# Kernel tuning notes

Hardware: AMD Instinct MI355X
Metric: run time of the kernel (lower is better)

## Reference

```python
import jax, jax.numpy as jnp
import numpy as np

B, S, E, H = 16, 256, 4096, 16
D = E // H  # 256; module's matmul pattern requires S == D and B == H


def setup_inputs() -> dict:
    rng = jax.random.key(0)
    k0, k1, k2, k3, k4 = jax.random.split(rng, 5)
    return {
        "query": jax.random.normal(k0, (B, S, E), jnp.float32),
        "key": jax.random.normal(k1, (B, S, E), jnp.float32),
        "value": jax.random.normal(k2, (B, S, E), jnp.float32),
        # out_proj: torch nn.Linear(E, E) -> y = x @ W.T + b
        "out_w": jax.random.normal(k3, (E, E), jnp.float32) * 0.02,
        "out_b": jnp.zeros((E,), jnp.float32),
    }


def reference(query, key, value, out_w, out_b):
    scale = D ** -0.5
    # split heads: [B, S, E] -> [B, H, S, D]
    q = (query * scale).reshape(B, S, H, D).transpose(0, 2, 1, 3)
    k = key.reshape(B, S, H, D).transpose(0, 2, 1, 3)
    v = value.reshape(B, S, H, D).transpose(0, 2, 1, 3)
    # torch.matmul(q_head, k_head) with NO transpose: contracts q's D with k's S
    # (valid because S == D). aw: [B, H, S, D]
    aw = jnp.einsum('bhit,bhtj->bhij', q, k)
    # attn_weights.transpose(0, 1): [B, H, ...] -> [H, B, ...]
    aw = jnp.swapaxes(aw, 0, 1)
    # eval mode path: softmax over last dim (no dropout)
    aw = jax.nn.softmax(aw, axis=-1)
    # torch.matmul(aw [H,B,S,D], v [B,H,S,D]): batch dims broadcast because B == H,
    # pairing elementwise -> out[x,y] = aw[x,y] @ v[x,y]
    out = jnp.einsum('xyit,xytj->xyij', aw, v)
    # transpose(1, 2) then reshape to (B, S, E)
    out = jnp.swapaxes(out, 1, 2).reshape(B, S, E)
    # out_proj
    return out @ out_w.T + out_b
```

## Files before the change

kernel.cpp:

```cpp
#include <hip/hip_runtime.h>

#define AS1 __attribute__((address_space(1)))
#define AS3 __attribute__((address_space(3)))

typedef __bf16 bf16x8 __attribute__((ext_vector_type(8)));
typedef float f32x4 __attribute__((ext_vector_type(4)));

__device__ __forceinline__ unsigned short f2bf(float f) {
  unsigned int u = __builtin_bit_cast(unsigned int, f);
  u += 0x7fffu + ((u >> 16) & 1u);
  return (unsigned short)(u >> 16);
}

__global__ __launch_bounds__(256) void kv_transpose(
    const float* __restrict__ key, const float* __restrict__ value,
    unsigned short* __restrict__ KT2, unsigned short* __restrict__ VT2) {
  __shared__ float tr[32 * 33];
  const int tid = threadIdx.x;
  const int ts  = blockIdx.y;
  const int pp  = blockIdx.x >> 3;
  const int s   = blockIdx.x & 7;
  const int b   = ts ? (pp >> 4) : (pp & 15);
  const int h   = ts ? (pp & 15) : (pp >> 4);
  const float* src = (ts ? value : key) + ((size_t)(b * 256 + s * 32)) * 4096 + h * 256;
  unsigned short* dst = (ts ? VT2 : KT2) + (size_t)(pp * 8 + s) * 8192;
  const int tt = tid >> 3;
  const int q8 = tid & 7;
  for (int jb = 0; jb < 8; ++jb) {
    float4 v = *(const float4*)(src + (size_t)tt * 4096 + jb * 32 + q8 * 4);
    tr[tt * 33 + q8 * 4 + 0] = v.x;
    tr[tt * 33 + q8 * 4 + 1] = v.y;
    tr[tt * 33 + q8 * 4 + 2] = v.z;
    tr[tt * 33 + q8 * 4 + 3] = v.w;
    __syncthreads();
    ushort4 o;
    o.x = f2bf(tr[(q8 * 4 + 0) * 33 + tt]);
    o.y = f2bf(tr[(q8 * 4 + 1) * 33 + tt]);
    o.z = f2bf(tr[(q8 * 4 + 2) * 33 + tt]);
    o.w = f2bf(tr[(q8 * 4 + 3) * 33 + tt]);
    *(ushort4*)(dst + (jb * 32 + tt) * 32 + q8 * 4) = o;
    __syncthreads();
  }
}

__global__ __launch_bounds__(256, 2) void attn_kernel(
    const float* __restrict__ qin, const unsigned short* __restrict__ KT2,
    const unsigned short* __restrict__ VT2, unsigned short* __restrict__ attn) {
  __shared__ __align__(16) unsigned short kv[8192];
  __shared__ __align__(16) unsigned short plds[4 * 16 * 264];

  const int tid  = threadIdx.x;
  const int lane = tid & 63;
  const int wave = tid >> 6;
  const int li   = lane & 15;
  const int ks   = lane >> 4;

  const int bid = blockIdx.x;
  const int pp  = (bid & 7) * 32 + ((bid >> 3) & 31);
  const int ib  = bid >> 8;
  const int x = pp >> 4, y = pp & 15;
  const int i0 = ib * 64 + wave * 16;

  bf16x8 qf[8];
  {
    const float* qrow = qin + ((size_t)(y * 256 + i0 + li)) * 4096 + x * 256 + ks * 8;
#pragma unroll
    for (int s = 0; s < 8; ++s) {
      float4 v0 = *(const float4*)(qrow + s * 32);
      float4 v1 = *(const float4*)(qrow + s * 32 + 4);
      union { bf16x8 v; unsigned short u[8]; } t;
      t.u[0] = f2bf(v0.x * 0.0625f); t.u[1] = f2bf(v0.y * 0.0625f);
      t.u[2] = f2bf(v0.z * 0.0625f); t.u[3] = f2bf(v0.w * 0.0625f);
      t.u[4] = f2bf(v1.x * 0.0625f); t.u[5] = f2bf(v1.y * 0.0625f);
      t.u[6] = f2bf(v1.z * 0.0625f); t.u[7] = f2bf(v1.w * 0.0625f);
      qf[s] = t.v;
    }
  }

  const f32x4 vzero = {0.f, 0.f, 0.f, 0.f};
  f32x4 sacc[16];
#pragma unroll
  for (int f = 0; f < 16; ++f) sacc[f] = vzero;

  const unsigned short* ktile = KT2 + (size_t)pp * 65536;
#pragma unroll
  for (int s = 0; s < 8; ++s) {
    __syncthreads();
#pragma unroll
    for (int cc = 0; cc < 4; ++cc) {
      const unsigned short* g = ktile + (size_t)s * 8192 + (cc * 256 + tid) * 8;
      __builtin_amdgcn_global_load_lds((AS1 unsigned int*)g,
          (AS3 unsigned int*)((AS3 char*)kv + cc * 4096 + wave * 1024), 16, 0, 0);
    }
    __syncthreads();
#pragma unroll
    for (int f = 0; f < 16; ++f) {
      bf16x8 bfr = *(const bf16x8*)&kv[(f * 16 + li) * 32 + ks * 8];
      sacc[f] = __builtin_amdgcn_mfma_f32_16x16x32_bf16(qf[s], bfr, sacc[f], 0, 0, 0);
    }
  }

  float sm[4];
#pragma unroll
  for (int qi = 0; qi < 4; ++qi) {
    float m = sacc[0][qi];
#pragma unroll
    for (int f = 1; f < 16; ++f) m = fmaxf(m, sacc[f][qi]);
    m = fmaxf(m, __shfl_xor(m, 1));
    m = fmaxf(m, __shfl_xor(m, 2));
    m = fmaxf(m, __shfl_xor(m, 4));
    m = fmaxf(m, __shfl_xor(m, 8));
    float ssum = 0.f;
#pragma unroll
    for (int f = 0; f < 16; ++f) {
      float pv = __expf(sacc[f][qi] - m);
      sacc[f][qi] = pv;
      ssum += pv;
    }
    ssum += __shfl_xor(ssum, 1);
    ssum += __shfl_xor(ssum, 2);
    ssum += __shfl_xor(ssum, 4);
    ssum += __shfl_xor(ssum, 8);
    sm[qi] = ssum;
  }

  unsigned short* pw = plds + wave * 4224;
#pragma unroll
  for (int f = 0; f < 16; ++f)
#pragma unroll
    for (int qi = 0; qi < 4; ++qi)
      pw[(ks * 4 + qi) * 264 + f * 16 + li] = f2bf(sacc[f][qi]);

  f32x4 oacc[16];
#pragma unroll
  for (int f = 0; f < 16; ++f) oacc[f] = vzero;
  const unsigned short* vtile = VT2 + (size_t)pp * 65536;
  const unsigned short* pr = plds + wave * 4224 + li * 264;
#pragma unroll
  for (int s2 = 0; s2 < 8; ++s2) {
    __syncthreads();
#pragma unroll
    for (int cc = 0; cc < 4; ++cc) {
      const unsigned short* g = vtile + (size_t)s2 * 8192 + (cc * 256 + tid) * 8;
      __builtin_amdgcn_global_load_lds((AS1 unsigned int*)g,
          (AS3 unsigned int*)((AS3 char*)kv + cc * 4096 + wave * 1024), 16, 0, 0);
    }
    __syncthreads();
    bf16x8 afr = *(const bf16x8*)&pr[s2 * 32 + ks * 8];
#pragma unroll
    for (int f = 0; f < 16; ++f) {
      bf16x8 bfr = *(const bf16x8*)&kv[(f * 16 + li) * 32 + ks * 8];
      oacc[f] = __builtin_amdgcn_mfma_f32_16x16x32_bf16(afr, bfr, oacc[f], 0, 0, 0);
    }
  }

  float rs4[4];
#pragma unroll
  for (int qi = 0; qi < 4; ++qi) rs4[qi] = 1.0f / sm[qi];
  unsigned short* abase = attn + (size_t)(x * 256 + i0 + ks * 4) * 4096 + y * 256 + li;
#pragma unroll
  for (int f = 0; f < 16; ++f)
#pragma unroll
    for (int qi = 0; qi < 4; ++qi)
      abase[(size_t)qi * 4096 + f * 16] = f2bf(oacc[f][qi] * rs4[qi]);
}

__global__ __launch_bounds__(256) void convw(const float* __restrict__ w,
                                             unsigned short* __restrict__ o) {
  const int i = blockIdx.x * 256 + threadIdx.x;
  const float4* s = (const float4*)w + (size_t)i * 2;
  float4 v0 = s[0], v1 = s[1];
  uint4 pk;
  pk.x = (unsigned)f2bf(v0.x) | ((unsigned)f2bf(v0.y) << 16);
  pk.y = (unsigned)f2bf(v0.z) | ((unsigned)f2bf(v0.w) << 16);
  pk.z = (unsigned)f2bf(v1.x) | ((unsigned)f2bf(v1.y) << 16);
  pk.w = (unsigned)f2bf(v1.z) | ((unsigned)f2bf(v1.w) << 16);
  *((uint4*)o + i) = pk;
}

__global__ __launch_bounds__(256, 2) void proj_gemm(
    const unsigned short* __restrict__ A, const unsigned short* __restrict__ W,
    const float* __restrict__ bias, float* __restrict__ out) {
  __shared__ __align__(16) unsigned short As[4096];
  __shared__ __align__(16) unsigned short Bs[4096];
  const int tid  = threadIdx.x;
  const int lane = tid & 63;
  const int wave = tid >> 6;
  const int li   = lane & 15;
  const int ks   = lane >> 4;
  const int wr = wave >> 1, wc = wave & 1;

  const int bid = blockIdx.x;
  const int swz = (bid & 7) * 128 + (bid >> 3);
  const int m0 = (swz >> 5) * 128, n0 = (swz & 31) * 128;

  const f32x4 vzero = {0.f, 0.f, 0.f, 0.f};
  f32x4 acc[4][4];
#pragma unroll
  for (int m = 0; m < 4; ++m)
#pragma unroll
    for (int n = 0; n < 4; ++n) acc[m][n] = vzero;

  const char* a0 = (const char*)A + (size_t)(m0 + (tid >> 2)) * 8192 + (tid & 3) * 16;
  const char* a1 = a0 + (size_t)64 * 8192;
  const char* b0 = (const char*)W + (size_t)(n0 + (tid >> 2)) * 8192 + (tid & 3) * 16;
  const char* b1 = b0 + (size_t)64 * 8192;
  AS3 unsigned int* lA0 = (AS3 unsigned int*)((AS3 char*)As + wave * 1024);
  AS3 unsigned int* lA1 = (AS3 unsigned int*)((AS3 char*)As + 4096 + wave * 1024);
  AS3 unsigned int* lB0 = (AS3 unsigned int*)((AS3 char*)Bs + wave * 1024);
  AS3 unsigned int* lB1 = (AS3 unsigned int*)((AS3 char*)Bs + 4096 + wave * 1024);

  for (int kt = 0; kt < 128; ++kt) {
    __builtin_amdgcn_global_load_lds((AS1 unsigned int*)(a0 + kt * 64), lA0, 16, 0, 0);
    __builtin_amdgcn_global_load_lds((AS1 unsigned int*)(a1 + kt * 64), lA1, 16, 0, 0);
    __builtin_amdgcn_global_load_lds((AS1 unsigned int*)(b0 + kt * 64), lB0, 16, 0, 0);
    __builtin_amdgcn_global_load_lds((AS1 unsigned int*)(b1 + kt * 64), lB1, 16, 0, 0);
    __syncthreads();
    bf16x8 af[4], bf[4];
#pragma unroll
    for (int m = 0; m < 4; ++m)
      af[m] = *(const bf16x8*)&As[(wr * 64 + m * 16 + li) * 32 + ks * 8];
#pragma unroll
    for (int n = 0; n < 4; ++n)
      bf[n] = *(const bf16x8*)&Bs[(wc * 64 + n * 16 + li) * 32 + ks * 8];
#pragma unroll
    for (int m = 0; m < 4; ++m)
#pragma unroll
      for (int n = 0; n < 4; ++n)
        acc[m][n] = __builtin_amdgcn_mfma_f32_16x16x32_bf16(af[m], bf[n], acc[m][n], 0, 0, 0);
    __syncthreads();
  }

  float bv[4];
#pragma unroll
  for (int n = 0; n < 4; ++n) bv[n] = bias[n0 + wc * 64 + n * 16 + li];
#pragma unroll
  for (int m = 0; m < 4; ++m) {
#pragma unroll
    for (int qi = 0; qi < 4; ++qi) {
      const int row = m0 + wr * 64 + m * 16 + ks * 4 + qi;
      float* orow = out + (size_t)row * 4096 + n0 + wc * 64 + li;
#pragma unroll
      for (int n = 0; n < 4; ++n) orow[n * 16] = acc[m][n][qi] + bv[n];
    }
  }
}

extern "C" void kernel_launch(void* const* d_in, const int* in_sizes, int n_in,
                              void* d_out, int out_size, void* d_ws, size_t ws_size,
                              hipStream_t stream) {
  const float* q = (const float*)d_in[0];
  const float* k = (const float*)d_in[1];
  const float* v = (const float*)d_in[2];
  const float* w = (const float*)d_in[3];
  const float* b = (const float*)d_in[4];
  float* out = (float*)d_out;
  char* ws = (char*)d_ws;

  unsigned short* attn = (unsigned short*)ws;
  unsigned short* KT2  = (unsigned short*)(ws + (size_t)33554432);
  unsigned short* VT2  = (unsigned short*)(ws + (size_t)67108864);
  unsigned short* wbf  = KT2;

  kv_transpose<<<dim3(2048, 2), 256, 0, stream>>>(k, v, KT2, VT2);
  attn_kernel<<<1024, 256, 0, stream>>>(q, KT2, VT2, attn);
  convw<<<8192, 256, 0, stream>>>(w, wbf);
  proj_gemm<<<1024, 256, 0, stream>>>(attn, wbf, b, out);
}
```

Measured before the change: 276.2 us.

## Rewrite output projection GEMM as 256x256 tile, 8-wave, double-buffered pipeline

Replaces the 128x128, 4-wave projection GEMM with a 256x256-tile, 8-wave kernel. It uses a 128 KB LDS double buffer with async global-to-LDS prefetch two k-steps ahead, an XOR-swizzled LDS layout to avoid bank conflicts, and interleaves MFMA phases with staged loads under s_setprio. The goal is to raise arithmetic intensity and hide global load latency behind compute. The trade-offs are fewer blocks (256 on the device), heavy LDS use, and fragile manual waitcnt and barrier choreography.

```diff
diff --git a/kernel.cpp b/kernel.cpp
--- a/kernel.cpp
+++ b/kernel.cpp
@@ -178,72 +178,175 @@
   *((uint4*)o + i) = pk;
 }
 
-__global__ __launch_bounds__(256, 2) void proj_gemm(
+__global__ __launch_bounds__(512, 2) void proj_gemm8(
     const unsigned short* __restrict__ A, const unsigned short* __restrict__ W,
     const float* __restrict__ bias, float* __restrict__ out) {
-  __shared__ __align__(16) unsigned short As[4096];
-  __shared__ __align__(16) unsigned short Bs[4096];
+  __shared__ __align__(1024) char lds[131072];
+
   const int tid  = threadIdx.x;
   const int lane = tid & 63;
-  const int wave = tid >> 6;
+  const int w    = tid >> 6;
   const int li   = lane & 15;
   const int ks   = lane >> 4;
-  const int wr = wave >> 1, wc = wave & 1;
+  const int wr   = w >> 2;
+  const int wc   = w & 3;
+  const int LB   = (li * 64 + ks * 16) ^ (((li >> 3) & 1) << 5);
 
   const int bid = blockIdx.x;
-  const int swz = (bid & 7) * 128 + (bid >> 3);
-  const int m0 = (swz >> 5) * 128, n0 = (swz & 31) * 128;
+  const int swz = (bid & 7) * 32 + (bid >> 3);
+  const int m0b = (swz >> 4) * 256, n0b = (swz & 15) * 256;
+
+  unsigned sA[2][2], sB[2][2];
+#pragma unroll
+  for (int i2 = 0; i2 < 2; ++i2) {
+    int P = w * 2048 + i2 * 1024 + lane * 16;
+    int L = P ^ (((P >> 9) & 1) << 5);
+    int kk = L >> 13, row = (L >> 6) & 127, cb = L & 63;
+#pragma unroll
+    for (int h = 0; h < 2; ++h) {
+      sA[h][i2] = (unsigned)((m0b + h * 128 + row) * 8192 + kk * 64 + cb);
+      sB[h][i2] = (unsigned)((n0b + h * 128 + row) * 8192 + kk * 64 + cb);
+    }
+  }
+  const char* Ac = (const char*)A;
+  const char* Wc = (const char*)W;
+  AS3 char* L3 = (AS3 char*)lds;
 
   const f32x4 vzero = {0.f, 0.f, 0.f, 0.f};
-  f32x4 acc[4][4];
-#pragma unroll
-  for (int m = 0; m < 4; ++m)
+  f32x4 acc[8][4];
+#pragma unroll
+  for (int m = 0; m < 8; ++m)
 #pragma unroll
     for (int n = 0; n < 4; ++n) acc[m][n] = vzero;
 
-  const char* a0 = (const char*)A + (size_t)(m0 + (tid >> 2)) * 8192 + (tid & 3) * 16;
-  const char* a1 = a0 + (size_t)64 * 8192;
-  const char* b0 = (const char*)W + (size_t)(n0 + (tid >> 2)) * 8192 + (tid & 3) * 16;
-  const char* b1 = b0 + (size_t)64 * 8192;
-  AS3 unsigned int* lA0 = (AS3 unsigned int*)((AS3 char*)As + wave * 1024);
-  AS3 unsigned int* lA1 = (AS3 unsigned int*)((AS3 char*)As + 4096 + wave * 1024);
-  AS3 unsigned int* lB0 = (AS3 unsigned int*)((AS3 char*)Bs + wave * 1024);
-  AS3 unsigned int* lB1 = (AS3 unsigned int*)((AS3 char*)Bs + 4096 + wave * 1024);
-
-  for (int kt = 0; kt < 128; ++kt) {
-    __builtin_amdgcn_global_load_lds((AS1 unsigned int*)(a0 + kt * 64), lA0, 16, 0, 0);
-    __builtin_amdgcn_global_load_lds((AS1 unsigned int*)(a1 + kt * 64), lA1, 16, 0, 0);
-    __builtin_amdgcn_global_load_lds((AS1 unsigned int*)(b0 + kt * 64), lB0, 16, 0, 0);
-    __builtin_amdgcn_global_load_lds((AS1 unsigned int*)(b1 + kt * 64), lB1, 16, 0, 0);
-    __syncthreads();
-    bf16x8 af[4], bf[4];
-#pragma unroll
-    for (int m = 0; m < 4; ++m)
-      af[m] = *(const bf16x8*)&As[(wr * 64 + m * 16 + li) * 32 + ks * 8];
-#pragma unroll
-    for (int n = 0; n < 4; ++n)
-      bf[n] = *(const bf16x8*)&Bs[(wc * 64 + n * 16 + li) * 32 + ks * 8];
-#pragma unroll
-    for (int m = 0; m < 4; ++m)
-#pragma unroll
-      for (int n = 0; n < 4; ++n)
-        acc[m][n] = __builtin_amdgcn_mfma_f32_16x16x32_bf16(af[m], bf[n], acc[m][n], 0, 0, 0);
-    __syncthreads();
+#define STAGE_A(h, i2, koffb, bufo) \
+  __builtin_amdgcn_global_load_lds((AS1 unsigned int*)(Ac + sA[h][i2] + (koffb)), \
+      (AS3 unsigned int*)(L3 + (bufo) + (h) * 16384 + w * 2048 + (i2) * 1024), 16, 0, 0)
+#define STAGE_B(h, i2, koffb, bufo) \
+  __builtin_amdgcn_global_load_lds((AS1 unsigned int*)(Wc + sB[h][i2] + (koffb)), \
+      (AS3 unsigned int*)(L3 + 65536 + (bufo) + (h) * 16384 + w * 2048 + (i2) * 1024), 16, 0, 0)
+#define RD_A(m, kk) (*(const bf16x8*)(lds + aoff + wr * 16384 + (kk) * 8192 + (m) * 1024 + LB))
+#define RD_B(n, kk) (*(const bf16x8*)(lds + boff + (wc >> 1) * 16384 + (kk) * 8192 + \
+                                      (wc & 1) * 4096 + (n) * 1024 + LB))
+#define MFMA(a, b, c) __builtin_amdgcn_mfma_f32_16x16x32_bf16((a), (b), (c), 0, 0, 0)
+
+#pragma unroll
+  for (int tt = 0; tt < 2; ++tt) {
+#pragma unroll
+    for (int h = 0; h < 2; ++h)
+#pragma unroll
+      for (int i2 = 0; i2 < 2; ++i2) {
+        STAGE_A(h, i2, tt * 128u, tt * 32768);
+        STAGE_B(h, i2, tt * 128u, tt * 32768);
+      }
+  }
+  asm volatile("s_waitcnt vmcnt(8)" ::: "memory");
+  __builtin_amdgcn_s_barrier();
+
+  bf16x8 afr[4][2], bA[2][2], bB[2][2];
+
+  for (int t = 0; t < 64; ++t) {
+    const int cur  = t & 1;
+    const int aoff = cur * 32768;
+    const int boff = 65536 + cur * 32768;
+    const int ts   = (t + 2 < 64) ? t + 2 : 63;
+    const unsigned koff = (unsigned)ts * 128u;
+
+#pragma unroll
+    for (int m = 0; m < 4; ++m)
+#pragma unroll
+      for (int kk = 0; kk < 2; ++kk) afr[m][kk] = RD_A(m, kk);
+#pragma unroll
+    for (int n = 0; n < 2; ++n)
+#pragma unroll
+      for (int kk = 0; kk < 2; ++kk) bA[n][kk] = RD_B(n, kk);
+    __builtin_amdgcn_s_barrier();
+    asm volatile("s_waitcnt lgkmcnt(0)" ::: "memory");
+    __builtin_amdgcn_s_setprio(1);
+#pragma unroll
+    for (int m = 0; m < 4; ++m)
+#pragma unroll
+      for (int n = 0; n < 2; ++n)
+#pragma unroll
+        for (int kk = 0; kk < 2; ++kk)
+          acc[m][n] = MFMA(afr[m][kk], bA[n][kk], acc[m][n]);
+    __builtin_amdgcn_s_setprio(0);
+    __builtin_amdgcn_s_barrier();
+
+#pragma unroll
+    for (int n = 0; n < 2; ++n)
+#pragma unroll
+      for (int kk = 0; kk < 2; ++kk) bB[n][kk] = RD_B(n + 2, kk);
+    __builtin_amdgcn_s_barrier();
+    asm volatile("s_waitcnt lgkmcnt(0)" ::: "memory");
+    __builtin_amdgcn_s_setprio(1);
+#pragma unroll
+    for (int m = 0; m < 4; ++m)
+#pragma unroll
+      for (int n = 0; n < 2; ++n)
+#pragma unroll
+        for (int kk = 0; kk < 2; ++kk)
+          acc[m][n + 2] = MFMA(afr[m][kk], bB[n][kk], acc[m][n + 2]);
+    __builtin_amdgcn_s_setprio(0);
+    __builtin_amdgcn_s_barrier();
+
+#pragma unroll
+    for (int m = 0; m < 4; ++m)
+#pragma unroll
+      for (int kk = 0; kk < 2; ++kk) afr[m][kk] = RD_A(m + 4, kk);
+#pragma unroll
+    for (int h = 0; h < 2; ++h)
+#pragma unroll
+      for (int i2 = 0; i2 < 2; ++i2) STAGE_B(h, i2, koff, aoff);
+    __builtin_amdgcn_s_barrier();
+    asm volatile("s_waitcnt lgkmcnt(0)" ::: "memory");
+    __builtin_amdgcn_s_setprio(1);
+#pragma unroll
+    for (int m = 0; m < 4; ++m)
+#pragma unroll
+      for (int n = 0; n < 2; ++n)
+#pragma unroll
+        for (int kk = 0; kk < 2; ++kk)
+          acc[m + 4][n + 2] = MFMA(afr[m][kk], bB[n][kk], acc[m + 4][n + 2]);
+    __builtin_amdgcn_s_setprio(0);
+    __builtin_amdgcn_s_barrier();
+
+#pragma unroll
+    for (int h = 0; h < 2; ++h)
+#pragma unroll
+      for (int i2 = 0; i2 < 2; ++i2) STAGE_A(h, i2, koff, aoff);
+    __builtin_amdgcn_s_barrier();
+    __builtin_amdgcn_s_setprio(1);
+#pragma unroll
+    for (int m = 0; m < 4; ++m)
+#pragma unroll
+      for (int n = 0; n < 2; ++n)
+#pragma unroll
+        for (int kk = 0; kk < 2; ++kk)
+          acc[m + 4][n] = MFMA(afr[m][kk], bA[n][kk], acc[m + 4][n]);
+    __builtin_amdgcn_s_setprio(0);
+    asm volatile("s_waitcnt vmcnt(8)" ::: "memory");
+    __builtin_amdgcn_s_barrier();
   }
 
   float bv[4];
 #pragma unroll
-  for (int n = 0; n < 4; ++n) bv[n] = bias[n0 + wc * 64 + n * 16 + li];
-#pragma unroll
-  for (int m = 0; m < 4; ++m) {
+  for (int n = 0; n < 4; ++n) bv[n] = bias[n0b + wc * 64 + n * 16 + li];
+#pragma unroll
+  for (int m = 0; m < 8; ++m) {
 #pragma unroll
     for (int qi = 0; qi < 4; ++qi) {
-      const int row = m0 + wr * 64 + m * 16 + ks * 4 + qi;
-      float* orow = out + (size_t)row * 4096 + n0 + wc * 64 + li;
+      const int row = m0b + wr * 128 + m * 16 + ks * 4 + qi;
+      float* orow = out + (size_t)row * 4096 + n0b + wc * 64 + li;
 #pragma unroll
       for (int n = 0; n < 4; ++n) orow[n * 16] = acc[m][n][qi] + bv[n];
     }
   }
+#undef STAGE_A
+#undef STAGE_B
+#undef RD_A
+#undef RD_B
+#undef MFMA
 }
 
 extern "C" void kernel_launch(void* const* d_in, const int* in_sizes, int n_in,
@@ -265,5 +368,5 @@
   kv_transpose<<<dim3(2048, 2), 256, 0, stream>>>(k, v, KT2, VT2);
   attn_kernel<<<1024, 256, 0, stream>>>(q, KT2, VT2, attn);
   convw<<<8192, 256, 0, stream>>>(w, wbf);
-  proj_gemm<<<1024, 256, 0, stream>>>(attn, wbf, b, out);
-}
+  proj_gemm8<<<256, 512, 0, stream>>>(attn, wbf, b, out);
+}
```

Measured after the change: 237.4 us. -14.0%, faster.

## Rewrite projection GEMM with 256x256 tiles, 4-stage LDS pipeline and swizzled layout

Applied to the files above, without the earlier changes.

Replaces the 128x128 single-buffered projection GEMM with a 512-thread kernel that computes 256x256 output tiles per block. Global-to-LDS loads run through a 4-slot ring buffer prefetching three K-steps ahead, with explicit waitcnt/barrier scheduling and s_setprio around the MFMA bursts. LDS reads use an XOR swizzle to avoid bank conflicts. The goal is to hide memory latency and raise arithmetic intensity. The cost is 128KB of LDS per block and only 256 blocks, which limits occupancy, and the hand-written waitcnt counts are fragile.

```diff
diff --git a/kernel.cpp b/kernel.cpp
--- a/kernel.cpp
+++ b/kernel.cpp
@@ -178,72 +178,119 @@
   *((uint4*)o + i) = pk;
 }
 
-__global__ __launch_bounds__(256, 2) void proj_gemm(
+__global__ __launch_bounds__(512, 2) void proj_gemm8(
     const unsigned short* __restrict__ A, const unsigned short* __restrict__ W,
     const float* __restrict__ bias, float* __restrict__ out) {
-  __shared__ __align__(16) unsigned short As[4096];
-  __shared__ __align__(16) unsigned short Bs[4096];
+  __shared__ __align__(1024) char lds[131072];
+
   const int tid  = threadIdx.x;
   const int lane = tid & 63;
-  const int wave = tid >> 6;
+  const int w    = tid >> 6;
   const int li   = lane & 15;
   const int ks   = lane >> 4;
-  const int wr = wave >> 1, wc = wave & 1;
+  const int wr   = w >> 2;
+  const int wc   = w & 3;
+  const int LB   = li * 64 + ((ks * 16) ^ ((((li >> 1) & 3)) << 4));
 
   const int bid = blockIdx.x;
-  const int swz = (bid & 7) * 128 + (bid >> 3);
-  const int m0 = (swz >> 5) * 128, n0 = (swz & 31) * 128;
+  const int swz = (bid & 7) * 32 + (bid >> 3);
+  const int m0b = (swz >> 4) * 256, n0b = (swz & 15) * 256;
+
+  unsigned srcA[2], srcB[2];
+  int dstP[2];
+#pragma unroll
+  for (int j = 0; j < 2; ++j) {
+    int P = tid * 16 + j * 8192;
+    int L = P ^ ((P >> 3) & 0x30);
+    int row = L >> 6, col = L & 63;
+    srcA[j] = (unsigned)((m0b + row) * 8192 + col);
+    srcB[j] = (unsigned)((n0b + row) * 8192 + col);
+    dstP[j] = P;
+  }
+  const char* Ac = (const char*)A;
+  const char* Wc = (const char*)W;
+  AS3 char* L3 = (AS3 char*)lds;
 
   const f32x4 vzero = {0.f, 0.f, 0.f, 0.f};
-  f32x4 acc[4][4];
-#pragma unroll
-  for (int m = 0; m < 4; ++m)
+  f32x4 acc[8][4];
+#pragma unroll
+  for (int m = 0; m < 8; ++m)
 #pragma unroll
     for (int n = 0; n < 4; ++n) acc[m][n] = vzero;
 
-  const char* a0 = (const char*)A + (size_t)(m0 + (tid >> 2)) * 8192 + (tid & 3) * 16;
-  const char* a1 = a0 + (size_t)64 * 8192;
-  const char* b0 = (const char*)W + (size_t)(n0 + (tid >> 2)) * 8192 + (tid & 3) * 16;
-  const char* b1 = b0 + (size_t)64 * 8192;
-  AS3 unsigned int* lA0 = (AS3 unsigned int*)((AS3 char*)As + wave * 1024);
-  AS3 unsigned int* lA1 = (AS3 unsigned int*)((AS3 char*)As + 4096 + wave * 1024);
-  AS3 unsigned int* lB0 = (AS3 unsigned int*)((AS3 char*)Bs + wave * 1024);
-  AS3 unsigned int* lB1 = (AS3 unsigned int*)((AS3 char*)Bs + 4096 + wave * 1024);
-
-  for (int kt = 0; kt < 128; ++kt) {
-    __builtin_amdgcn_global_load_lds((AS1 unsigned int*)(a0 + kt * 64), lA0, 16, 0, 0);
-    __builtin_amdgcn_global_load_lds((AS1 unsigned int*)(a1 + kt * 64), lA1, 16, 0, 0);
-    __builtin_amdgcn_global_load_lds((AS1 unsigned int*)(b0 + kt * 64), lB0, 16, 0, 0);
-    __builtin_amdgcn_global_load_lds((AS1 unsigned int*)(b1 + kt * 64), lB1, 16, 0, 0);
-    __syncthreads();
-    bf16x8 af[4], bf[4];
-#pragma unroll
-    for (int m = 0; m < 4; ++m)
-      af[m] = *(const bf16x8*)&As[(wr * 64 + m * 16 + li) * 32 + ks * 8];
-#pragma unroll
-    for (int n = 0; n < 4; ++n)
-      bf[n] = *(const bf16x8*)&Bs[(wc * 64 + n * 16 + li) * 32 + ks * 8];
-#pragma unroll
-    for (int m = 0; m < 4; ++m)
-#pragma unroll
-      for (int n = 0; n < 4; ++n)
-        acc[m][n] = __builtin_amdgcn_mfma_f32_16x16x32_bf16(af[m], bf[n], acc[m][n], 0, 0, 0);
-    __syncthreads();
+#define STAGE(T) do {                                                          \
+    const int _sl = ((T) & 3) * 32768; const unsigned _ko = (unsigned)(T) * 64u; \
+    _Pragma("unroll") for (int j = 0; j < 2; ++j) {                            \
+      __builtin_amdgcn_global_load_lds((AS1 unsigned int*)(Ac + srcA[j] + _ko),\
+          (AS3 unsigned int*)(L3 + _sl + dstP[j]), 16, 0, 0);                  \
+      __builtin_amdgcn_global_load_lds((AS1 unsigned int*)(Wc + srcB[j] + _ko),\
+          (AS3 unsigned int*)(L3 + _sl + 16384 + dstP[j]), 16, 0, 0);          \
+    } } while (0)
+#define RD_A(S, M) (*(const bf16x8*)(lds + (S) + wr * 8192 + (M) * 1024 + LB))
+#define RD_B(S, N) (*(const bf16x8*)(lds + (S) + 16384 + wc * 4096 + (N) * 1024 + LB))
+#define MFMA(a, b, c) __builtin_amdgcn_mfma_f32_16x16x32_bf16((a), (b), (c), 0, 0, 0)
+
+  bf16x8 A0[4], A1[4], Bc[4], Bn[4];
+
+  STAGE(0); STAGE(1); STAGE(2);
+  asm volatile("s_waitcnt vmcnt(4)" ::: "memory");
+  __builtin_amdgcn_s_barrier();
+#pragma unroll
+  for (int m = 0; m < 4; ++m) A0[m] = RD_A(0, m);
+#pragma unroll
+  for (int n = 0; n < 4; ++n) Bc[n] = RD_B(0, n);
+
+#define TILE(T, BU, BN2) do {                                                  \
+    const int cs = ((T) & 3) * 32768;                                          \
+    const int ns = (((T) + 1) & 3) * 32768;                                    \
+    const int ss = ((T) + 3 < 128) ? (T) + 3 : 127;                            \
+    _Pragma("unroll") for (int m = 0; m < 4; ++m) A1[m] = RD_A(cs, m + 4);     \
+    _Pragma("unroll") for (int n = 0; n < 4; ++n) BN2[n] = RD_B(ns, n);        \
+    STAGE(ss);                                                                 \
+    __builtin_amdgcn_s_barrier();                                              \
+    asm volatile("s_waitcnt lgkmcnt(8)" ::: "memory");                         \
+    __builtin_amdgcn_s_setprio(1);                                             \
+    _Pragma("unroll") for (int m = 0; m < 4; ++m)                              \
+      _Pragma("unroll") for (int n = 0; n < 4; ++n)                            \
+        acc[m][n] = MFMA(A0[m], BU[n], acc[m][n]);                             \
+    __builtin_amdgcn_s_setprio(0);                                             \
+    asm volatile("s_waitcnt vmcnt(8)" ::: "memory");                           \
+    __builtin_amdgcn_s_barrier();                                              \
+    _Pragma("unroll") for (int m = 0; m < 4; ++m) A0[m] = RD_A(ns, m);         \
+    __builtin_amdgcn_s_barrier();                                              \
+    asm volatile("s_waitcnt lgkmcnt(8)" ::: "memory");                         \
+    __builtin_amdgcn_s_setprio(1);                                             \
+    _Pragma("unroll") for (int m = 0; m < 4; ++m)                              \
+      _Pragma("unroll") for (int n = 0; n < 4; ++n)                            \
+        acc[m + 4][n] = MFMA(A1[m], BU[n], acc[m + 4][n]);                     \
+    __builtin_amdgcn_s_setprio(0);                                             \
+    asm volatile("s_waitcnt vmcnt(4)" ::: "memory");                           \
+    __builtin_amdgcn_s_barrier();                                              \
+  } while (0)
+
+  for (int it = 0; it < 64; ++it) {
+    TILE(2 * it,     Bc, Bn);
+    TILE(2 * it + 1, Bn, Bc);
   }
 
   float bv[4];
 #pragma unroll
-  for (int n = 0; n < 4; ++n) bv[n] = bias[n0 + wc * 64 + n * 16 + li];
-#pragma unroll
-  for (int m = 0; m < 4; ++m) {
+  for (int n = 0; n < 4; ++n) bv[n] = bias[n0b + wc * 64 + n * 16 + li];
+#pragma unroll
+  for (int m = 0; m < 8; ++m) {
 #pragma unroll
     for (int qi = 0; qi < 4; ++qi) {
-      const int row = m0 + wr * 64 + m * 16 + ks * 4 + qi;
-      float* orow = out + (size_t)row * 4096 + n0 + wc * 64 + li;
+      const int row = m0b + wr * 128 + m * 16 + ks * 4 + qi;
+      float* orow = out + (size_t)row * 4096 + n0b + wc * 64 + li;
 #pragma unroll
       for (int n = 0; n < 4; ++n) orow[n * 16] = acc[m][n][qi] + bv[n];
     }
   }
+#undef STAGE
+#undef RD_A
+#undef RD_B
+#undef MFMA
+#undef TILE
 }
 
 extern "C" void kernel_launch(void* const* d_in, const int* in_sizes, int n_in,
@@ -265,5 +312,5 @@
   kv_transpose<<<dim3(2048, 2), 256, 0, stream>>>(k, v, KT2, VT2);
   attn_kernel<<<1024, 256, 0, stream>>>(q, KT2, VT2, attn);
   convw<<<8192, 256, 0, stream>>>(w, wbf);
-  proj_gemm<<<1024, 256, 0, stream>>>(attn, wbf, b, out);
-}
+  proj_gemm8<<<256, 512, 0, stream>>>(attn, wbf, b, out);
+}
```

After: 238.8 us. 13.5% less time.
